# Kernel tuning notes

Measured on AMD Instinct MI355X. Metric: run time of the kernel, lower is better.

## Reference

```python
import jax, jax.numpy as jnp
import numpy as np

N = 100000      # num graph nodes
E = 1600000     # num edges (avg degree 16)
IN = 128        # in_channels
H = 128         # hidden_channels
B = 4096        # query batch
CTX = 20        # context set length (indices[:, 3:])


def setup_inputs() -> dict:
    key = jax.random.key(0)
    ks = jax.random.split(key, 16)
    inp = {
        "indices": jax.random.randint(ks[0], (B, 3 + CTX), 0, N, dtype=jnp.int64),
        "src": jax.random.randint(ks[1], (E,), 0, N, dtype=jnp.int32),
        "dst": jax.random.randint(ks[2], (E,), 0, N, dtype=jnp.int32),
        "w": jax.random.uniform(ks[3], (E,), dtype=jnp.float32),
        # learned params
        "ndata": jax.random.normal(ks[4], (N, IN), dtype=jnp.float32),
        "W1": jax.random.normal(ks[5], (H, IN), dtype=jnp.float32) * (1.0 / np.sqrt(IN)),
        "b1": jnp.zeros((H,), jnp.float32),
        "W2": jax.random.normal(ks[6], (H, H), dtype=jnp.float32) * (1.0 / np.sqrt(H)),
        "b2": jnp.zeros((H,), jnp.float32),
        "eps": jnp.zeros((2,), jnp.float32),  # learn_eps, one per GINConv
        "Wc1": jax.random.normal(ks[7], (H, 3 * H), dtype=jnp.float32) * (1.0 / np.sqrt(3 * H)),
        "bc1": jnp.zeros((H,), jnp.float32),
        "Wc2": jax.random.normal(ks[8], (H // 2, H), dtype=jnp.float32) * (1.0 / np.sqrt(H)),
        "bc2": jnp.zeros((H // 2,), jnp.float32),
        "Wc3": jax.random.normal(ks[9], (1, H // 2), dtype=jnp.float32) * (1.0 / np.sqrt(H // 2)),
        "bc3": jnp.zeros((1,), jnp.float32),
    }
    return inp


def _gin_conv(x, src, dst, w, deg, eps, W, b):
    # DGL GINConv(mean, learn_eps): h = lin((1+eps)*x + mean_{in-edges}(w_e * x_src))
    msg = w[:, None] * x[src]                                   # [E, D]
    agg = jax.ops.segment_sum(msg, dst, num_segments=N) / deg   # [N, D]
    return ((1.0 + eps) * x + agg) @ W.T + b


def reference(indices, src, dst, w, ndata, W1, b1, W2, b2, eps,
              Wc1, bc1, Wc2, bc2, Wc3, bc3):
    deg = jax.ops.segment_sum(jnp.ones((E,), ndata.dtype), dst, num_segments=N)
    deg = jnp.maximum(deg, 1.0)[:, None]

    x = ndata
    x = jax.nn.relu(_gin_conv(x, src, dst, w, deg, eps[0], W1, b1))  # dropout inactive (eval)
    x = _gin_conv(x, src, dst, w, deg, eps[1], W2, b2)               # last layer: no relu
    x = x.at[0].set(0.0)                                             # x[0] = zeros

    ing1 = x[indices[:, 0]]   # [B, H]
    ing2 = x[indices[:, 1]]   # [B, H]

    # embed_context: mean over nonzero-index context members
    ctx_idx = indices[:, 3:]                                   # [B, CTX]
    ctx_sum = x[ctx_idx].sum(axis=1)                           # [B, H]
    norm = jnp.maximum((ctx_idx > 0).sum(axis=1), 1).astype(x.dtype)[:, None]
    ctx = ctx_sum / norm

    y = jnp.concatenate([ing1, ing2, ctx], axis=1)             # [B, 3H]
    y = jax.nn.relu(y @ Wc1.T + bc1)
    y = jax.nn.relu(y @ Wc2.T + bc2)
    y = y @ Wc3.T + bc3                                        # [B, 1]
    return y
```

## Files before the change

kernel.cpp:

```cpp
#include <hip/hip_runtime.h>


#define CONV_NPB 32

__global__ void prep_transpose(const float* __restrict__ W1, const float* __restrict__ W2,
                               const float* __restrict__ Wc1, const float* __restrict__ Wc2,
                               float* __restrict__ Wt1, float* __restrict__ Wt2,
                               float* __restrict__ Wc1t, float* __restrict__ Wc2t) {
  int i = blockIdx.x * blockDim.x + threadIdx.x;
  if (i < 16384) {
    int f = i >> 7, k = i & 127;
    Wt1[k * 128 + f] = W1[i];
  } else if (i < 32768) {
    int j = i - 16384; int f = j >> 7, k = j & 127;
    Wt2[k * 128 + f] = W2[j];
  } else if (i < 81920) {
    int j = i - 32768; int f = j / 384, k = j % 384;
    Wc1t[k * 128 + f] = Wc1[j];
  } else if (i < 90112) {
    int j = i - 81920; int f = j >> 7, k = j & 127;
    Wc2t[k * 64 + f] = Wc2[j];
  }
}

__global__ void hist_kernel(const int* __restrict__ dst, int* __restrict__ cnt,
                            int* __restrict__ rank, int E) {
  int e = blockIdx.x * blockDim.x + threadIdx.x;
  if (e < E) rank[e] = atomicAdd(&cnt[dst[e]], 1);
}

__global__ void scan1_kernel(const int* __restrict__ cnt, int* __restrict__ prow,
                             int* __restrict__ bsum, int n) {
  __shared__ int smem[256];
  const int t = threadIdx.x;
  const int base = blockIdx.x * 2048 + t * 8;
  int v[8];
  int s = 0;
#pragma unroll
  for (int j = 0; j < 8; ++j) {
    int idx = base + j;
    v[j] = (idx < n) ? ((cnt[idx] + 7) & ~7) : 0;
    s += v[j];
  }
  smem[t] = s;
  __syncthreads();
  for (int off = 1; off < 256; off <<= 1) {
    int add = (t >= off) ? smem[t - off] : 0;
    __syncthreads();
    smem[t] += add;
    __syncthreads();
  }
  int run = smem[t] - s;
  if (t == 255) bsum[blockIdx.x] = smem[255];
#pragma unroll
  for (int j = 0; j < 8; ++j) {
    int idx = base + j;
    if (idx < n) prow[idx] = run;
    run += v[j];
  }
}

__global__ void scan2_kernel(int* __restrict__ bsum, int nb) {
  const int t = threadIdx.x;
  if (nb <= 64) {
    const int orig = (t < nb) ? bsum[t] : 0;
    int v = orig;
#pragma unroll
    for (int off = 1; off < 64; off <<= 1) {
      int u = __shfl_up(v, off);
      if (t >= off) v += u;
    }
    if (t == nb - 1) bsum[nb] = v;
    if (t < nb) bsum[t] = v - orig;
  } else if (t == 0) {
    int run = 0;
    for (int i = 0; i < nb; ++i) { int v = bsum[i]; bsum[i] = run; run += v; }
    bsum[nb] = run;
  }
}

__global__ void scan3_kernel(int* __restrict__ prow, const int* __restrict__ bsum,
                             int n, int nchunk) {
  int i = blockIdx.x * blockDim.x + threadIdx.x;
  if (i < n) prow[i] += bsum[i >> 11];
  if (i == 0) prow[n] = bsum[nchunk];
}

__global__ void scatter_kernel(const int* __restrict__ src, const int* __restrict__ dst,
                               const float* __restrict__ w, const int* __restrict__ prow,
                               const int* __restrict__ rank, int2* __restrict__ epack, int E) {
  int e = blockIdx.x * blockDim.x + threadIdx.x;
  if (e < E) {
    int pos = prow[dst[e]] + rank[e];
    epack[pos] = make_int2(src[e], __float_as_int(w[e]));
  }
}

__launch_bounds__(256, 6)
__global__ void conv_kernel(const float* __restrict__ xin, float* __restrict__ xout,
                            const int* __restrict__ prow, const int* __restrict__ cnt,
                            const int2* __restrict__ epack,
                            const float* __restrict__ Wt,
                            const float* __restrict__ bias, const float* __restrict__ eps,
                            int epsidx, int dorelu, int zerorow0, int n) {
  __shared__ float xm[CONV_NPB * 128];
  __shared__ int rp_s[CONV_NPB + 1];
  const int t = threadIdx.x;
  const int nb = blockIdx.x * CONV_NPB;
  const float epsv = 1.0f + eps[epsidx];

#pragma unroll
  for (int i = 0; i < 4; ++i)
    *(float4*)&xm[(t + i * 256) * 4] = make_float4(0.f, 0.f, 0.f, 0.f);
  if (t <= CONV_NPB) {
    int node = nb + t;
    rp_s[t] = prow[node <= n ? node : n];
  }
  __syncthreads();

  {
    const int L = t >> 5;
    const int lane = t & 31;
    const int f0 = lane * 4;
    const int e0 = rp_s[0], eT = rp_s[CONV_NPB];
    const int nbat = (eT - e0) >> 3;
    const int chunk = (((nbat + 7) >> 3)) << 3;
    const int jb = e0 + L * chunk;
    const int je = min(jb + chunk, eT);
    if (jb < je) {
      const int4* ep4 = (const int4*)epack;
      int r = 0;
      while (rp_s[r + 1] <= jb) ++r;
      float4 acc = make_float4(0.f, 0.f, 0.f, 0.f);
      for (int j = jb; j < je; j += 8) {
        if (rp_s[r + 1] <= j) {
          float* bp = &xm[r * 128 + lane];
          atomicAdd(bp + 0,  acc.x);
          atomicAdd(bp + 32, acc.y);
          atomicAdd(bp + 64, acc.z);
          atomicAdd(bp + 96, acc.w);
          acc = make_float4(0.f, 0.f, 0.f, 0.f);
          do { ++r; } while (rp_s[r + 1] <= j);
        }
        const int h = j >> 1;
        const int4 q0 = ep4[h + 0];
        const int4 q1 = ep4[h + 1];
        const int4 q2 = ep4[h + 2];
        const int4 q3 = ep4[h + 3];
        const float4 a0 = *(const float4*)&xin[(size_t)q0.x * 128 + f0];
        const float4 a1 = *(const float4*)&xin[(size_t)q0.z * 128 + f0];
        const float4 a2 = *(const float4*)&xin[(size_t)q1.x * 128 + f0];
        const float4 a3 = *(const float4*)&xin[(size_t)q1.z * 128 + f0];
        const float4 a4 = *(const float4*)&xin[(size_t)q2.x * 128 + f0];
        const float4 a5 = *(const float4*)&xin[(size_t)q2.z * 128 + f0];
        const float4 a6 = *(const float4*)&xin[(size_t)q3.x * 128 + f0];
        const float4 a7 = *(const float4*)&xin[(size_t)q3.z * 128 + f0];
        const float w0 = __int_as_float(q0.y), w1 = __int_as_float(q0.w);
        const float w2 = __int_as_float(q1.y), w3 = __int_as_float(q1.w);
        const float w4 = __int_as_float(q2.y), w5 = __int_as_float(q2.w);
        const float w6 = __int_as_float(q3.y), w7 = __int_as_float(q3.w);
        acc.x += w0 * a0.x + w1 * a1.x + w2 * a2.x + w3 * a3.x
               + w4 * a4.x + w5 * a5.x + w6 * a6.x + w7 * a7.x;
        acc.y += w0 * a0.y + w1 * a1.y + w2 * a2.y + w3 * a3.y
               + w4 * a4.y + w5 * a5.y + w6 * a6.y + w7 * a7.y;
        acc.z += w0 * a0.z + w1 * a1.z + w2 * a2.z + w3 * a3.z
               + w4 * a4.z + w5 * a5.z + w6 * a6.z + w7 * a7.z;
        acc.w += w0 * a0.w + w1 * a1.w + w2 * a2.w + w3 * a3.w
               + w4 * a4.w + w5 * a5.w + w6 * a6.w + w7 * a7.w;
      }
      float* bp = &xm[r * 128 + lane];
      atomicAdd(bp + 0,  acc.x);
      atomicAdd(bp + 32, acc.y);
      atomicAdd(bp + 64, acc.z);
      atomicAdd(bp + 96, acc.w);
    }
  }
  __syncthreads();

  {
    float4 m[4];
#pragma unroll
    for (int q = 0; q < 4; ++q) {
      const int task = t + q * 256;
      const int r = task >> 5;
      const int fg = task & 31;
      m[q].x = xm[r * 128 + fg];
      m[q].y = xm[r * 128 + 32 + fg];
      m[q].z = xm[r * 128 + 64 + fg];
      m[q].w = xm[r * 128 + 96 + fg];
    }
    __syncthreads();
#pragma unroll
    for (int q = 0; q < 4; ++q) {
      const int task = t + q * 256;
      const int r = task >> 5;
      const int fg = task & 31;
      const int f0 = fg * 4;
      const int node = nb + r;
      float4 v = make_float4(0.f, 0.f, 0.f, 0.f);
      if (node < n) {
        const int d = cnt[node];
        const float rdeg = 1.0f / (float)(d > 1 ? d : 1);
        const float4 xv = *(const float4*)&xin[(size_t)node * 128 + f0];
        v.x = epsv * xv.x + m[q].x * rdeg;
        v.y = epsv * xv.y + m[q].y * rdeg;
        v.z = epsv * xv.z + m[q].z * rdeg;
        v.w = epsv * xv.w + m[q].w * rdeg;
      }
      *(float4*)&xm[r * 128 + f0] = v;
    }
  }
  __syncthreads();

  {
    const int fg = t & 31;
    const int rg = t >> 5;
    const int f0 = fg * 4;
    const int r0 = rg * 4;
    float4 acc[4];
#pragma unroll
    for (int r = 0; r < 4; ++r) acc[r] = make_float4(0.f, 0.f, 0.f, 0.f);
    for (int k = 0; k < 128; k += 4) {
      const float4 w0 = *(const float4*)&Wt[(k + 0) * 128 + f0];
      const float4 w1 = *(const float4*)&Wt[(k + 1) * 128 + f0];
      const float4 w2 = *(const float4*)&Wt[(k + 2) * 128 + f0];
      const float4 w3 = *(const float4*)&Wt[(k + 3) * 128 + f0];
#pragma unroll
      for (int r = 0; r < 4; ++r) {
        const float4 xv = *(const float4*)&xm[(r0 + r) * 128 + k];
        acc[r].x += xv.x * w0.x + xv.y * w1.x + xv.z * w2.x + xv.w * w3.x;
        acc[r].y += xv.x * w0.y + xv.y * w1.y + xv.z * w2.y + xv.w * w3.y;
        acc[r].z += xv.x * w0.z + xv.y * w1.z + xv.z * w2.z + xv.w * w3.z;
        acc[r].w += xv.x * w0.w + xv.y * w1.w + xv.z * w2.w + xv.w * w3.w;
      }
    }
    const float4 bv = *(const float4*)&bias[f0];
#pragma unroll
    for (int r = 0; r < 4; ++r) {
      const int node = nb + r0 + r;
      if (node < n) {
        float4 v;
        v.x = acc[r].x + bv.x;
        v.y = acc[r].y + bv.y;
        v.z = acc[r].z + bv.z;
        v.w = acc[r].w + bv.w;
        if (dorelu) {
          v.x = fmaxf(v.x, 0.f); v.y = fmaxf(v.y, 0.f);
          v.z = fmaxf(v.z, 0.f); v.w = fmaxf(v.w, 0.f);
        }
        if (zerorow0 && node == 0) { v.x = 0.f; v.y = 0.f; v.z = 0.f; v.w = 0.f; }
        *(float4*)&xout[(size_t)node * 128 + f0] = v;
      }
    }
  }
}

__launch_bounds__(128, 4)
__global__ void final_kernel(const float* __restrict__ x2, const int* __restrict__ indices,
                             const float* __restrict__ Wc1t, const float* __restrict__ bc1,
                             const float* __restrict__ Wc2t, const float* __restrict__ bc2,
                             const float* __restrict__ Wc3, const float* __restrict__ bc3,
                             float* __restrict__ out) {
  __shared__ float ysm[384];
  __shared__ float h1s[128];
  const int b = blockIdx.x;
  const int t = threadIdx.x;
  const int* ind = indices + (size_t)b * 23;

  {
    const int i0 = ind[0];
    const int i1 = ind[1];
    ysm[t] = x2[(size_t)i0 * 128 + t];
    ysm[128 + t] = x2[(size_t)i1 * 128 + t];
    float cs = 0.f;
    int cc = 0;
#pragma unroll
    for (int j = 0; j < 20; ++j) {
      const int cj = ind[3 + j];
      cc += (cj > 0) ? 1 : 0;
      cs += x2[(size_t)cj * 128 + t];
    }
    ysm[256 + t] = cs / (float)(cc > 0 ? cc : 1);
  }
  __syncthreads();

  {
    float acc = bc1[t];
    for (int k = 0; k < 384; k += 4) {
      const float4 yv = *(const float4*)&ysm[k];
      acc += yv.x * Wc1t[(k + 0) * 128 + t];
      acc += yv.y * Wc1t[(k + 1) * 128 + t];
      acc += yv.z * Wc1t[(k + 2) * 128 + t];
      acc += yv.w * Wc1t[(k + 3) * 128 + t];
    }
    h1s[t] = fmaxf(acc, 0.f);
  }
  __syncthreads();

  if (t < 64) {
    float acc = bc2[t];
    for (int k = 0; k < 128; k += 4) {
      const float4 hv = *(const float4*)&h1s[k];
      acc += hv.x * Wc2t[(k + 0) * 64 + t];
      acc += hv.y * Wc2t[(k + 1) * 64 + t];
      acc += hv.z * Wc2t[(k + 2) * 64 + t];
      acc += hv.w * Wc2t[(k + 3) * 64 + t];
    }
    float v = fmaxf(acc, 0.f) * Wc3[t];
#pragma unroll
    for (int o = 32; o > 0; o >>= 1) v += __shfl_down(v, o);
    if (t == 0) out[b] = v + bc3[0];
  }
}

extern "C" void kernel_launch(void* const* d_in, const int* in_sizes, int n_in,
                              void* d_out, int out_size, void* d_ws, size_t ws_size,
                              hipStream_t stream) {
  const int* indices = (const int*)d_in[0];
  const int* src = (const int*)d_in[1];
  const int* dst = (const int*)d_in[2];
  const float* w = (const float*)d_in[3];
  const float* ndata = (const float*)d_in[4];
  const float* W1 = (const float*)d_in[5];
  const float* b1 = (const float*)d_in[6];
  const float* W2 = (const float*)d_in[7];
  const float* b2 = (const float*)d_in[8];
  const float* eps = (const float*)d_in[9];
  const float* Wc1 = (const float*)d_in[10];
  const float* bc1 = (const float*)d_in[11];
  const float* Wc2 = (const float*)d_in[12];
  const float* bc2 = (const float*)d_in[13];
  const float* Wc3 = (const float*)d_in[14];
  const float* bc3 = (const float*)d_in[15];
  float* out = (float*)d_out;

  const int E = in_sizes[1];
  const int N = in_sizes[4] / 128;
  const int B = in_sizes[0] / 23;

  char* ws = (char*)d_ws;
  size_t off = 0;
  auto alloc = [&](size_t bytes) -> char* {
    char* p = ws + off;
    off = (off + bytes + 255) & ~(size_t)255;
    return p;
  };
  const size_t Epad = (size_t)E + 8 * (size_t)N;
  int* cnt = (int*)alloc((size_t)N * 4);
  int* prow = (int*)alloc((size_t)(N + 1) * 4);
  int* rank = (int*)alloc((size_t)E * 4);
  int* bsum = (int*)alloc(256 * 4);
  int2* epack = (int2*)alloc(Epad * 8);
  float* x1 = (float*)alloc((size_t)N * 128 * 4);
  float* x2 = (float*)alloc((size_t)N * 128 * 4);
  float* Wt1 = (float*)alloc(16384 * 4);
  float* Wt2 = (float*)alloc(16384 * 4);
  float* Wc1t = (float*)alloc(49152 * 4);
  float* Wc2t = (float*)alloc(8192 * 4);

  hipMemsetAsync(cnt, 0, (size_t)N * 4, stream);
  hipMemsetAsync(epack, 0, Epad * 8, stream);

  prep_transpose<<<(90112 + 255) / 256, 256, 0, stream>>>(W1, W2, Wc1, Wc2, Wt1, Wt2, Wc1t, Wc2t);
  hist_kernel<<<(E + 255) / 256, 256, 0, stream>>>(dst, cnt, rank, E);
  const int nchunk = (N + 2047) / 2048;
  scan1_kernel<<<nchunk, 256, 0, stream>>>(cnt, prow, bsum, N);
  scan2_kernel<<<1, 64, 0, stream>>>(bsum, nchunk);
  scan3_kernel<<<(N + 255) / 256, 256, 0, stream>>>(prow, bsum, N, nchunk);
  scatter_kernel<<<(E + 255) / 256, 256, 0, stream>>>(src, dst, w, prow, rank, epack, E);

  const int nconv = (N + CONV_NPB - 1) / CONV_NPB;
  conv_kernel<<<nconv, 256, 0, stream>>>(ndata, x1, prow, cnt, epack, Wt1, b1, eps, 0, 1, 0, N);
  conv_kernel<<<nconv, 256, 0, stream>>>(x1, x2, prow, cnt, epack, Wt2, b2, eps, 1, 0, 1, N);

  final_kernel<<<B, 128, 0, stream>>>(x2, indices, Wc1t, bc1, Wc2t, bc2, Wc3, bc3, out);
}
```

Measured before the change: 607.0 us.

## Gather with full 64-lane wavefronts per edge and batch 16 queries per final block

The conv gather now gives each 64-lane wavefront a single edge stream, with each lane loading a float2 of features. Edge indices and weights are made wave-uniform with readfirstlane, and occupancy is raised to 8 blocks. The combine step no longer stages values through registers with an extra barrier. The final MLP kernel now handles 16 queries per 256-thread block so each Wc1/Wc2 weight load is reused across 8 or 4 rows, and context sums are split across two thread halves with shared-memory atomics. The risks are fewer bytes in flight per load and more edge batches per wave, and the higher occupancy bound may force register spills.

Result: slower. 727.1 us (+19.8%).

```diff
diff --git a/kernel.cpp b/kernel.cpp
--- a/kernel.cpp
+++ b/kernel.cpp
@@ -96,7 +96,7 @@
   }
 }
 
-__launch_bounds__(256, 6)
+__launch_bounds__(256, 8)
 __global__ void conv_kernel(const float* __restrict__ xin, float* __restrict__ xout,
                             const int* __restrict__ prow, const int* __restrict__ cnt,
                             const int2* __restrict__ epack,
@@ -119,27 +119,24 @@
   __syncthreads();
 
   {
-    const int L = t >> 5;
-    const int lane = t & 31;
-    const int f0 = lane * 4;
+    const int wvid = t >> 6;
+    const int lane = t & 63;
+    const int f0 = lane * 2;
     const int e0 = rp_s[0], eT = rp_s[CONV_NPB];
     const int nbat = (eT - e0) >> 3;
-    const int chunk = (((nbat + 7) >> 3)) << 3;
-    const int jb = e0 + L * chunk;
+    const int chunk = ((nbat + 3) >> 2) << 3;
+    const int jb = e0 + wvid * chunk;
     const int je = min(jb + chunk, eT);
     if (jb < je) {
       const int4* ep4 = (const int4*)epack;
       int r = 0;
       while (rp_s[r + 1] <= jb) ++r;
-      float4 acc = make_float4(0.f, 0.f, 0.f, 0.f);
+      float ax = 0.f, ay = 0.f;
       for (int j = jb; j < je; j += 8) {
         if (rp_s[r + 1] <= j) {
-          float* bp = &xm[r * 128 + lane];
-          atomicAdd(bp + 0,  acc.x);
-          atomicAdd(bp + 32, acc.y);
-          atomicAdd(bp + 64, acc.z);
-          atomicAdd(bp + 96, acc.w);
-          acc = make_float4(0.f, 0.f, 0.f, 0.f);
+          atomicAdd(&xm[r * 128 + f0], ax);
+          atomicAdd(&xm[r * 128 + f0 + 1], ay);
+          ax = 0.f; ay = 0.f;
           do { ++r; } while (rp_s[r + 1] <= j);
         }
         const int h = j >> 1;
@@ -147,67 +144,61 @@
         const int4 q1 = ep4[h + 1];
         const int4 q2 = ep4[h + 2];
         const int4 q3 = ep4[h + 3];
-        const float4 a0 = *(const float4*)&xin[(size_t)q0.x * 128 + f0];
-        const float4 a1 = *(const float4*)&xin[(size_t)q0.z * 128 + f0];
-        const float4 a2 = *(const float4*)&xin[(size_t)q1.x * 128 + f0];
-        const float4 a3 = *(const float4*)&xin[(size_t)q1.z * 128 + f0];
-        const float4 a4 = *(const float4*)&xin[(size_t)q2.x * 128 + f0];
-        const float4 a5 = *(const float4*)&xin[(size_t)q2.z * 128 + f0];
-        const float4 a6 = *(const float4*)&xin[(size_t)q3.x * 128 + f0];
-        const float4 a7 = *(const float4*)&xin[(size_t)q3.z * 128 + f0];
-        const float w0 = __int_as_float(q0.y), w1 = __int_as_float(q0.w);
-        const float w2 = __int_as_float(q1.y), w3 = __int_as_float(q1.w);
-        const float w4 = __int_as_float(q2.y), w5 = __int_as_float(q2.w);
-        const float w6 = __int_as_float(q3.y), w7 = __int_as_float(q3.w);
-        acc.x += w0 * a0.x + w1 * a1.x + w2 * a2.x + w3 * a3.x
-               + w4 * a4.x + w5 * a5.x + w6 * a6.x + w7 * a7.x;
-        acc.y += w0 * a0.y + w1 * a1.y + w2 * a2.y + w3 * a3.y
-               + w4 * a4.y + w5 * a5.y + w6 * a6.y + w7 * a7.y;
-        acc.z += w0 * a0.z + w1 * a1.z + w2 * a2.z + w3 * a3.z
-               + w4 * a4.z + w5 * a5.z + w6 * a6.z + w7 * a7.z;
-        acc.w += w0 * a0.w + w1 * a1.w + w2 * a2.w + w3 * a3.w
-               + w4 * a4.w + w5 * a5.w + w6 * a6.w + w7 * a7.w;
-      }
-      float* bp = &xm[r * 128 + lane];
-      atomicAdd(bp + 0,  acc.x);
-      atomicAdd(bp + 32, acc.y);
-      atomicAdd(bp + 64, acc.z);
-      atomicAdd(bp + 96, acc.w);
-    }
-  }
-  __syncthreads();
-
-  {
-    float4 m[4];
+        const int s0 = __builtin_amdgcn_readfirstlane(q0.x);
+        const int s1 = __builtin_amdgcn_readfirstlane(q0.z);
+        const int s2 = __builtin_amdgcn_readfirstlane(q1.x);
+        const int s3 = __builtin_amdgcn_readfirstlane(q1.z);
+        const int s4 = __builtin_amdgcn_readfirstlane(q2.x);
+        const int s5 = __builtin_amdgcn_readfirstlane(q2.z);
+        const int s6 = __builtin_amdgcn_readfirstlane(q3.x);
+        const int s7 = __builtin_amdgcn_readfirstlane(q3.z);
+        const float2 a0 = *(const float2*)&xin[(size_t)s0 * 128 + f0];
+        const float2 a1 = *(const float2*)&xin[(size_t)s1 * 128 + f0];
+        const float2 a2 = *(const float2*)&xin[(size_t)s2 * 128 + f0];
+        const float2 a3 = *(const float2*)&xin[(size_t)s3 * 128 + f0];
+        const float2 a4 = *(const float2*)&xin[(size_t)s4 * 128 + f0];
+        const float2 a5 = *(const float2*)&xin[(size_t)s5 * 128 + f0];
+        const float2 a6 = *(const float2*)&xin[(size_t)s6 * 128 + f0];
+        const float2 a7 = *(const float2*)&xin[(size_t)s7 * 128 + f0];
+        const float w0 = __uint_as_float(__builtin_amdgcn_readfirstlane(q0.y));
+        const float w1 = __uint_as_float(__builtin_amdgcn_readfirstlane(q0.w));
+        const float w2 = __uint_as_float(__builtin_amdgcn_readfirstlane(q1.y));
+        const float w3 = __uint_as_float(__builtin_amdgcn_readfirstlane(q1.w));
+        const float w4 = __uint_as_float(__builtin_amdgcn_readfirstlane(q2.y));
+        const float w5 = __uint_as_float(__builtin_amdgcn_readfirstlane(q2.w));
+        const float w6 = __uint_as_float(__builtin_amdgcn_readfirstlane(q3.y));
+        const float w7 = __uint_as_float(__builtin_amdgcn_readfirstlane(q3.w));
+        ax += w0 * a0.x + w1 * a1.x + w2 * a2.x + w3 * a3.x
+            + w4 * a4.x + w5 * a5.x + w6 * a6.x + w7 * a7.x;
+        ay += w0 * a0.y + w1 * a1.y + w2 * a2.y + w3 * a3.y
+            + w4 * a4.y + w5 * a5.y + w6 * a6.y + w7 * a7.y;
+      }
+      atomicAdd(&xm[r * 128 + f0], ax);
+      atomicAdd(&xm[r * 128 + f0 + 1], ay);
+    }
+  }
+  __syncthreads();
+
+  {
 #pragma unroll
     for (int q = 0; q < 4; ++q) {
       const int task = t + q * 256;
       const int r = task >> 5;
-      const int fg = task & 31;
-      m[q].x = xm[r * 128 + fg];
-      m[q].y = xm[r * 128 + 32 + fg];
-      m[q].z = xm[r * 128 + 64 + fg];
-      m[q].w = xm[r * 128 + 96 + fg];
-    }
-    __syncthreads();
-#pragma unroll
-    for (int q = 0; q < 4; ++q) {
-      const int task = t + q * 256;
-      const int r = task >> 5;
-      const int fg = task & 31;
-      const int f0 = fg * 4;
+      const int f0 = (task & 31) * 4;
       const int node = nb + r;
-      float4 v = make_float4(0.f, 0.f, 0.f, 0.f);
       if (node < n) {
         const int d = cnt[node];
         const float rdeg = 1.0f / (float)(d > 1 ? d : 1);
         const float4 xv = *(const float4*)&xin[(size_t)node * 128 + f0];
-        v.x = epsv * xv.x + m[q].x * rdeg;
-        v.y = epsv * xv.y + m[q].y * rdeg;
-        v.z = epsv * xv.z + m[q].z * rdeg;
-        v.w = epsv * xv.w + m[q].w * rdeg;
-      }
-      *(float4*)&xm[r * 128 + f0] = v;
+        float4 m = *(const float4*)&xm[r * 128 + f0];
+        m.x = epsv * xv.x + m.x * rdeg;
+        m.y = epsv * xv.y + m.y * rdeg;
+        m.z = epsv * xv.z + m.z * rdeg;
+        m.w = epsv * xv.w + m.w * rdeg;
+        *(float4*)&xm[r * 128 + f0] = m;
+      } else {
+        *(float4*)&xm[r * 128 + f0] = make_float4(0.f, 0.f, 0.f, 0.f);
+      }
     }
   }
   __syncthreads();
@@ -255,61 +246,117 @@
   }
 }
 
-__launch_bounds__(128, 4)
+__launch_bounds__(256, 4)
 __global__ void final_kernel(const float* __restrict__ x2, const int* __restrict__ indices,
                              const float* __restrict__ Wc1t, const float* __restrict__ bc1,
                              const float* __restrict__ Wc2t, const float* __restrict__ bc2,
                              const float* __restrict__ Wc3, const float* __restrict__ bc3,
                              float* __restrict__ out) {
-  __shared__ float ysm[384];
-  __shared__ float h1s[128];
-  const int b = blockIdx.x;
+  __shared__ float ysm[16 * 384];
+  __shared__ float h1s[16 * 128];
+  __shared__ float h2s[16 * 64];
+  __shared__ float ccs[16];
   const int t = threadIdx.x;
-  const int* ind = indices + (size_t)b * 23;
-
-  {
-    const int i0 = ind[0];
-    const int i1 = ind[1];
-    ysm[t] = x2[(size_t)i0 * 128 + t];
-    ysm[128 + t] = x2[(size_t)i1 * 128 + t];
-    float cs = 0.f;
+  const int b0 = blockIdx.x * 16;
+
+#pragma unroll
+  for (int q = 0; q < 8; ++q) {
+    const int s = t + q * 256;
+    ysm[(s >> 7) * 384 + 256 + (s & 127)] = 0.f;
+  }
+  if (t < 16) {
+    const int* ind = indices + (size_t)(b0 + t) * 23;
     int cc = 0;
 #pragma unroll
-    for (int j = 0; j < 20; ++j) {
-      const int cj = ind[3 + j];
-      cc += (cj > 0) ? 1 : 0;
-      cs += x2[(size_t)cj * 128 + t];
-    }
-    ysm[256 + t] = cs / (float)(cc > 0 ? cc : 1);
-  }
-  __syncthreads();
-
-  {
-    float acc = bc1[t];
+    for (int j = 0; j < 20; ++j) cc += (ind[3 + j] > 0) ? 1 : 0;
+    ccs[t] = 1.0f / (float)(cc > 0 ? cc : 1);
+  }
+  __syncthreads();
+
+  {
+    const int f = t & 127;
+    const int half = t >> 7;
+#pragma unroll 1
+    for (int e = 0; e < 16; ++e) {
+      const int* ind = indices + (size_t)(b0 + e) * 23;
+      const int ing = ind[half];
+      ysm[e * 384 + half * 128 + f] = x2[(size_t)ing * 128 + f];
+      float cs = 0.f;
+#pragma unroll
+      for (int j = 0; j < 10; ++j) {
+        const int cj = ind[3 + half * 10 + j];
+        cs += x2[(size_t)cj * 128 + f];
+      }
+      atomicAdd(&ysm[e * 384 + 256 + f], cs);
+    }
+  }
+  __syncthreads();
+#pragma unroll
+  for (int q = 0; q < 8; ++q) {
+    const int s = t + q * 256;
+    const int e = s >> 7;
+    ysm[e * 384 + 256 + (s & 127)] *= ccs[e];
+  }
+  __syncthreads();
+
+  {
+    const int f1 = t & 127;
+    const int eh = t >> 7;
+    float acc[8];
+    const float b = bc1[f1];
+#pragma unroll
+    for (int i = 0; i < 8; ++i) acc[i] = b;
     for (int k = 0; k < 384; k += 4) {
-      const float4 yv = *(const float4*)&ysm[k];
-      acc += yv.x * Wc1t[(k + 0) * 128 + t];
-      acc += yv.y * Wc1t[(k + 1) * 128 + t];
-      acc += yv.z * Wc1t[(k + 2) * 128 + t];
-      acc += yv.w * Wc1t[(k + 3) * 128 + t];
-    }
-    h1s[t] = fmaxf(acc, 0.f);
-  }
-  __syncthreads();
-
-  if (t < 64) {
-    float acc = bc2[t];
+      const float wv0 = Wc1t[(k + 0) * 128 + f1];
+      const float wv1 = Wc1t[(k + 1) * 128 + f1];
+      const float wv2 = Wc1t[(k + 2) * 128 + f1];
+      const float wv3 = Wc1t[(k + 3) * 128 + f1];
+#pragma unroll
+      for (int i = 0; i < 8; ++i) {
+        const float4 yv = *(const float4*)&ysm[(eh * 8 + i) * 384 + k];
+        acc[i] += yv.x * wv0 + yv.y * wv1 + yv.z * wv2 + yv.w * wv3;
+      }
+    }
+#pragma unroll
+    for (int i = 0; i < 8; ++i)
+      h1s[(eh * 8 + i) * 128 + f1] = fmaxf(acc[i], 0.f);
+  }
+  __syncthreads();
+
+  {
+    const int f2 = t & 63;
+    const int eg = t >> 6;
+    float acc[4];
+    const float b = bc2[f2];
+#pragma unroll
+    for (int i = 0; i < 4; ++i) acc[i] = b;
     for (int k = 0; k < 128; k += 4) {
-      const float4 hv = *(const float4*)&h1s[k];
-      acc += hv.x * Wc2t[(k + 0) * 64 + t];
-      acc += hv.y * Wc2t[(k + 1) * 64 + t];
-      acc += hv.z * Wc2t[(k + 2) * 64 + t];
-      acc += hv.w * Wc2t[(k + 3) * 64 + t];
-    }
-    float v = fmaxf(acc, 0.f) * Wc3[t];
-#pragma unroll
-    for (int o = 32; o > 0; o >>= 1) v += __shfl_down(v, o);
-    if (t == 0) out[b] = v + bc3[0];
+      const float wv0 = Wc2t[(k + 0) * 64 + f2];
+      const float wv1 = Wc2t[(k + 1) * 64 + f2];
+      const float wv2 = Wc2t[(k + 2) * 64 + f2];
+      const float wv3 = Wc2t[(k + 3) * 64 + f2];
+#pragma unroll
+      for (int i = 0; i < 4; ++i) {
+        const float4 hv = *(const float4*)&h1s[(eg * 4 + i) * 128 + k];
+        acc[i] += hv.x * wv0 + hv.y * wv1 + hv.z * wv2 + hv.w * wv3;
+      }
+    }
+#pragma unroll
+    for (int i = 0; i < 4; ++i)
+      h2s[(eg * 4 + i) * 64 + f2] = fmaxf(acc[i], 0.f);
+  }
+  __syncthreads();
+
+  {
+    const int e = t >> 4;
+    const int l = t & 15;
+    float p = 0.f;
+#pragma unroll
+    for (int k = 0; k < 4; ++k)
+      p += h2s[e * 64 + l + k * 16] * Wc3[l + k * 16];
+#pragma unroll
+    for (int o = 8; o > 0; o >>= 1) p += __shfl_down(p, o, 16);
+    if (l == 0) out[b0 + e] = p + bc3[0];
   }
 }
 
@@ -373,5 +420,5 @@
   conv_kernel<<<nconv, 256, 0, stream>>>(ndata, x1, prow, cnt, epack, Wt1, b1, eps, 0, 1, 0, N);
   conv_kernel<<<nconv, 256, 0, stream>>>(x1, x2, prow, cnt, epack, Wt2, b2, eps, 1, 0, 1, N);
 
-  final_kernel<<<B, 128, 0, stream>>>(x2, indices, Wc1t, bc1, Wc2t, bc2, Wc3, bc3, out);
-}
+  final_kernel<<<B / 16, 256, 0, stream>>>(x2, indices, Wc1t, bc1, Wc2t, bc2, Wc3, bc3, out);
+}
```
